# Kernel optimization log

Hardware: AMD Instinct MI355X
Metric: run time of the kernel (lower is better)

The kernel has to match this reference:

```python
import jax, jax.numpy as jnp
import numpy as np

B, T, I = 32768, 28, 28
H, C = 128, 10


def setup_inputs() -> dict:
    key = jax.random.key(0)
    ks = jax.random.split(key, 7)
    s_u = 1.0 / np.sqrt(I)
    s_w = 1.0 / np.sqrt(H)
    return {
        "x": jax.random.normal(ks[0], (B, T, I), dtype=jnp.float32),
        "U_w": jax.random.uniform(ks[1], (H, I), jnp.float32, -s_u, s_u),
        "U_b": jax.random.uniform(ks[2], (H,), jnp.float32, -s_u, s_u),
        "W_w": jax.random.uniform(ks[3], (H, H), jnp.float32, -s_w, s_w),
        "W_b": jax.random.uniform(ks[4], (H,), jnp.float32, -s_w, s_w),
        "V_w": jax.random.uniform(ks[5], (C, H), jnp.float32, -s_w, s_w),
        "V_b": jax.random.uniform(ks[6], (C,), jnp.float32, -s_w, s_w),
    }


def reference(x, U_w, U_b, W_w, W_b, V_w, V_b):
    # x: [B, T, I]. Precompute input projections for all timesteps at once
    # (one big GEMM), then scan the sequential recurrence on S.
    ux = jnp.einsum("bti,hi->tbh", x, U_w) + U_b  # [T, B, H]

    def step(S, ux_t):
        S = jnp.tanh(ux_t + S @ W_w.T + W_b)
        return S, None

    S0 = jnp.zeros((x.shape[0], W_w.shape[0]), dtype=x.dtype)
    S_final, _ = jax.lax.scan(step, S0, ux)
    return S_final @ V_w.T + V_b  # [B, C]
```

## Files before the change

kernel.cpp:

```cpp
#include <hip/hip_runtime.h>


#define T_STEPS 28
#define I_DIM   28
#define S_STRIDE 132

typedef __attribute__((ext_vector_type(4))) float f32x4;
typedef __attribute__((ext_vector_type(8))) short short8;

#define MFMA16 __builtin_amdgcn_mfma_f32_16x16x32_bf16

__device__ __forceinline__ unsigned short f2bf(float f) {
  unsigned u = __builtin_bit_cast(unsigned, f);
  u += 0x7FFFu + ((u >> 16) & 1u);
  return (unsigned short)(u >> 16);
}
__device__ __forceinline__ float bf2f(unsigned short s) {
  return __builtin_bit_cast(float, (unsigned)s << 16);
}

__device__ __forceinline__ short8 to_frag(f32x4 a, f32x4 b) {
  union { unsigned short u[8]; short8 v; } r;
#pragma unroll
  for (int j = 0; j < 4; ++j) { r.u[j] = f2bf(a[j]); r.u[j + 4] = f2bf(b[j]); }
  return r.v;
}

__device__ __forceinline__ short8 load_sfrag(const unsigned short* sp, int off) {
  union { uint2 d[2]; short8 v; } r;
  r.d[0] = *(const uint2*)(sp + off);
  r.d[1] = *(const uint2*)(sp + off + 4);
  return r.v;
}

__device__ __forceinline__ float fast_tanh(float z) {
  float e = __expf(2.0f * z);
#if __has_builtin(__builtin_amdgcn_rcpf)
  return 1.0f - 2.0f * __builtin_amdgcn_rcpf(e + 1.0f);
#else
  return 1.0f - 2.0f / (e + 1.0f);
#endif
}

__global__ __launch_bounds__(256, 2) void rnn_fused(
    const float* __restrict__ x,  const float* __restrict__ Uw,
    const float* __restrict__ Ub, const float* __restrict__ Ww,
    const float* __restrict__ Wb, const float* __restrict__ Vw,
    const float* __restrict__ Vb, float* __restrict__ out) {
  __shared__ unsigned short Sbuf[2][64 * S_STRIDE];

  const int tid  = threadIdx.x;
  const int w    = tid >> 6;
  const int lane = tid & 63;
  const int l15  = lane & 15;
  const int q    = lane >> 4;
  const int mrow = (w >> 1) * 64;
  const int ncol = (w & 1) * 32;
  const int b0   = blockIdx.x * 64;

  const f32x4 zero4 = {0.f, 0.f, 0.f, 0.f};

  short8 wfrag[4][4];
  short8 ufrag[4];
  f32x4  bias[4];
#pragma unroll
  for (int mt = 0; mt < 4; ++mt) {
    const int h = mrow + mt * 16 + l15;
    const float* wp = Ww + h * 128 + q * 8;
#pragma unroll
    for (int kt = 0; kt < 4; ++kt) {
      wfrag[mt][kt] = to_frag(*(const f32x4*)wp, *(const f32x4*)(wp + 4));
      wp += 32;
    }
    const float* up = Uw + h * I_DIM + q * 8;
    f32x4 u0 = *(const f32x4*)up;
    f32x4 u1 = zero4;
    if (q < 3) u1 = *(const f32x4*)(up + 4);
    ufrag[mt] = to_frag(u0, u1);
    const int hb = mrow + mt * 16 + q * 4;
    bias[mt] = *(const f32x4*)(Wb + hb) + *(const f32x4*)(Ub + hb);
  }

  const float* xptr[2];
#pragma unroll
  for (int nt = 0; nt < 2; ++nt)
    xptr[nt] = x + (size_t)(b0 + ncol + nt * 16 + l15) * (T_STEPS * I_DIM) + q * 8;

  int ro[2];
#pragma unroll
  for (int nt = 0; nt < 2; ++nt) ro[nt] = (ncol + nt * 16 + l15) * S_STRIDE;

  f32x4 acc[4][2];

  {
    f32x4 xa[2], xbv[2];
#pragma unroll
    for (int nt = 0; nt < 2; ++nt) {
      xa[nt] = *(const f32x4*)xptr[nt];
      xbv[nt] = zero4;
      if (q < 3) xbv[nt] = *(const f32x4*)(xptr[nt] + 4);
      xptr[nt] += I_DIM;
    }
    short8 xf0 = to_frag(xa[0], xbv[0]);
    short8 xf1 = to_frag(xa[1], xbv[1]);
#pragma unroll
    for (int mt = 0; mt < 4; ++mt) {
      acc[mt][0] = MFMA16(ufrag[mt], xf0, zero4, 0, 0, 0);
      acc[mt][1] = MFMA16(ufrag[mt], xf1, zero4, 0, 0, 0);
    }
    unsigned short* wp = &Sbuf[1][0];
#pragma unroll
    for (int mt = 0; mt < 4; ++mt)
#pragma unroll
      for (int nt = 0; nt < 2; ++nt) {
        f32x4 z = acc[mt][nt] + bias[mt];
        unsigned s0 = f2bf(fast_tanh(z[0]));
        unsigned s1 = f2bf(fast_tanh(z[1]));
        unsigned s2 = f2bf(fast_tanh(z[2]));
        unsigned s3 = f2bf(fast_tanh(z[3]));
        uint2 d; d.x = s0 | (s1 << 16); d.y = s2 | (s3 << 16);
        *(uint2*)(wp + ro[nt] + mrow + mt * 16 + q * 4) = d;
      }
  }
  __syncthreads();

#pragma unroll 1
  for (int t = 1; t < T_STEPS; ++t) {
    f32x4 xa[2], xbv[2];
#pragma unroll
    for (int nt = 0; nt < 2; ++nt) {
      xa[nt] = *(const f32x4*)xptr[nt];
      xbv[nt] = zero4;
      if (q < 3) xbv[nt] = *(const f32x4*)(xptr[nt] + 4);
      xptr[nt] += I_DIM;
    }

    const unsigned short* sp = &Sbuf[t & 1][0];
#pragma unroll
    for (int mt = 0; mt < 4; ++mt) { acc[mt][0] = zero4; acc[mt][1] = zero4; }

#pragma unroll
    for (int kt = 0; kt < 4; ++kt) {
      short8 s0 = load_sfrag(sp, ro[0] + kt * 32 + q * 8);
      short8 s1 = load_sfrag(sp, ro[1] + kt * 32 + q * 8);
#pragma unroll
      for (int mt = 0; mt < 4; ++mt) {
        acc[mt][0] = MFMA16(wfrag[mt][kt], s0, acc[mt][0], 0, 0, 0);
        acc[mt][1] = MFMA16(wfrag[mt][kt], s1, acc[mt][1], 0, 0, 0);
      }
    }

    short8 xf0 = to_frag(xa[0], xbv[0]);
    short8 xf1 = to_frag(xa[1], xbv[1]);
#pragma unroll
    for (int mt = 0; mt < 4; ++mt) {
      acc[mt][0] = MFMA16(ufrag[mt], xf0, acc[mt][0], 0, 0, 0);
      acc[mt][1] = MFMA16(ufrag[mt], xf1, acc[mt][1], 0, 0, 0);
    }

    unsigned short* wp = &Sbuf[(t + 1) & 1][0];
#pragma unroll
    for (int mt = 0; mt < 4; ++mt)
#pragma unroll
      for (int nt = 0; nt < 2; ++nt) {
        f32x4 z = acc[mt][nt] + bias[mt];
        unsigned s0 = f2bf(fast_tanh(z[0]));
        unsigned s1 = f2bf(fast_tanh(z[1]));
        unsigned s2 = f2bf(fast_tanh(z[2]));
        unsigned s3 = f2bf(fast_tanh(z[3]));
        uint2 d; d.x = s0 | (s1 << 16); d.y = s2 | (s3 << 16);
        *(uint2*)(wp + ro[nt] + mrow + mt * 16 + q * 4) = d;
      }
    __syncthreads();
  }

  {
    const unsigned short* sf = &Sbuf[0][0];
    const int r  = tid >> 2;
    const int c0 = tid & 3;
    const float* v0 = Vw + c0 * 128;
    const float* v1 = Vw + (c0 + 4) * 128;
    const float* v2 = Vw + ((c0 & 1) + 8) * 128;
    const unsigned short* srow = sf + r * S_STRIDE;
    float a0 = 0.f, a1 = 0.f, a2 = 0.f;
#pragma unroll 8
    for (int h = 0; h < 128; ++h) {
      float s = bf2f(srow[h]);
      a0 += s * v0[h];
      a1 += s * v1[h];
      a2 += s * v2[h];
    }
    float* op = out + (size_t)(b0 + r) * 10;
    op[c0]     = a0 + Vb[c0];
    op[c0 + 4] = a1 + Vb[c0 + 4];
    if (c0 < 2) op[c0 + 8] = a2 + Vb[c0 + 8];
  }
}

extern "C" void kernel_launch(void* const* d_in, const int* in_sizes, int n_in,
                              void* d_out, int out_size, void* d_ws, size_t ws_size,
                              hipStream_t stream) {
  const float* x  = (const float*)d_in[0];
  const float* Uw = (const float*)d_in[1];
  const float* Ub = (const float*)d_in[2];
  const float* Ww = (const float*)d_in[3];
  const float* Wb = (const float*)d_in[4];
  const float* Vw = (const float*)d_in[5];
  const float* Vb = (const float*)d_in[6];
  rnn_fused<<<512, 256, 0, stream>>>(x, Uw, Ub, Ww, Wb, Vw, Vb, (float*)d_out);
}
```

Baseline: 213.6 us.

## Halve batch tile per block, raise occupancy, use packed bf16 convert and exp2 tanh

Each block now handles 32 batch rows instead of 64 and the grid doubles to 1024 blocks. Launch bounds rise to 4 blocks per CU, so each wave issues fewer MFMAs per recurrence step, and more independent blocks are available to hide barrier and global-load latency. bf16 conversion switches to the packed cvt_pk builtin, tanh uses a vectorised exp2/rcp form, and the bias is folded into the accumulator initialisation. The cost is that the W fragments are reloaded per block for half as many rows, and the tighter register limit risks spills.

```diff
diff --git a/kernel.cpp b/kernel.cpp
--- a/kernel.cpp
+++ b/kernel.cpp
@@ -10,19 +10,29 @@
 
 #define MFMA16 __builtin_amdgcn_mfma_f32_16x16x32_bf16
 
-__device__ __forceinline__ unsigned short f2bf(float f) {
-  unsigned u = __builtin_bit_cast(unsigned, f);
-  u += 0x7FFFu + ((u >> 16) & 1u);
-  return (unsigned short)(u >> 16);
+__device__ __forceinline__ unsigned pack2(float lo, float hi) {
+#if __has_builtin(__builtin_amdgcn_cvt_pk_bf16_f32)
+  auto p = __builtin_amdgcn_cvt_pk_bf16_f32(lo, hi);
+  return __builtin_bit_cast(unsigned, p);
+#else
+  unsigned a = __builtin_bit_cast(unsigned, lo);
+  a += 0x7FFFu + ((a >> 16) & 1u);
+  unsigned b = __builtin_bit_cast(unsigned, hi);
+  b += 0x7FFFu + ((b >> 16) & 1u);
+  return (a >> 16) | (b & 0xFFFF0000u);
+#endif
 }
+
 __device__ __forceinline__ float bf2f(unsigned short s) {
   return __builtin_bit_cast(float, (unsigned)s << 16);
 }
 
 __device__ __forceinline__ short8 to_frag(f32x4 a, f32x4 b) {
-  union { unsigned short u[8]; short8 v; } r;
-#pragma unroll
-  for (int j = 0; j < 4; ++j) { r.u[j] = f2bf(a[j]); r.u[j + 4] = f2bf(b[j]); }
+  union { unsigned u[4]; short8 v; } r;
+  r.u[0] = pack2(a[0], a[1]);
+  r.u[1] = pack2(a[2], a[3]);
+  r.u[2] = pack2(b[0], b[1]);
+  r.u[3] = pack2(b[2], b[3]);
   return r.v;
 }
 
@@ -33,21 +43,25 @@
   return r.v;
 }
 
-__device__ __forceinline__ float fast_tanh(float z) {
-  float e = __expf(2.0f * z);
-#if __has_builtin(__builtin_amdgcn_rcpf)
-  return 1.0f - 2.0f * __builtin_amdgcn_rcpf(e + 1.0f);
-#else
-  return 1.0f - 2.0f / (e + 1.0f);
-#endif
+__device__ __forceinline__ f32x4 tanh4(f32x4 z) {
+  const float k = 2.8853900817779268f;
+  f32x4 t = z * k;
+  f32x4 e;
+#pragma unroll
+  for (int i = 0; i < 4; ++i) e[i] = __builtin_amdgcn_exp2f(t[i]);
+  f32x4 d = e + 1.0f;
+  f32x4 r;
+#pragma unroll
+  for (int i = 0; i < 4; ++i) r[i] = __builtin_amdgcn_rcpf(d[i]);
+  return 1.0f - 2.0f * r;
 }
 
-__global__ __launch_bounds__(256, 2) void rnn_fused(
+__global__ __launch_bounds__(256, 4) void rnn_fused(
     const float* __restrict__ x,  const float* __restrict__ Uw,
     const float* __restrict__ Ub, const float* __restrict__ Ww,
     const float* __restrict__ Wb, const float* __restrict__ Vw,
     const float* __restrict__ Vb, float* __restrict__ out) {
-  __shared__ unsigned short Sbuf[2][64 * S_STRIDE];
+  __shared__ __align__(16) unsigned short Sbuf[2][32 * S_STRIDE];
 
   const int tid  = threadIdx.x;
   const int w    = tid >> 6;
@@ -55,8 +69,8 @@
   const int l15  = lane & 15;
   const int q    = lane >> 4;
   const int mrow = (w >> 1) * 64;
-  const int ncol = (w & 1) * 32;
-  const int b0   = blockIdx.x * 64;
+  const int ncol = (w & 1) * 16;
+  const int b0   = blockIdx.x * 32;
 
   const f32x4 zero4 = {0.f, 0.f, 0.f, 0.f};
 
@@ -81,119 +95,79 @@
     bias[mt] = *(const f32x4*)(Wb + hb) + *(const f32x4*)(Ub + hb);
   }
 
-  const float* xptr[2];
-#pragma unroll
-  for (int nt = 0; nt < 2; ++nt)
-    xptr[nt] = x + (size_t)(b0 + ncol + nt * 16 + l15) * (T_STEPS * I_DIM) + q * 8;
+  const float* xlo = x + (size_t)(b0 + ncol + l15) * (T_STEPS * I_DIM) + q * 8;
+  const float* xhi = x + (size_t)(b0 + ncol + l15) * (T_STEPS * I_DIM)
+                       + ((q < 3) ? q * 8 + 4 : 0);
 
-  int ro[2];
-#pragma unroll
-  for (int nt = 0; nt < 2; ++nt) ro[nt] = (ncol + nt * 16 + l15) * S_STRIDE;
-
-  f32x4 acc[4][2];
+  const int ro = (ncol + l15) * S_STRIDE;
+  f32x4 acc[4];
 
   {
-    f32x4 xa[2], xbv[2];
-#pragma unroll
-    for (int nt = 0; nt < 2; ++nt) {
-      xa[nt] = *(const f32x4*)xptr[nt];
-      xbv[nt] = zero4;
-      if (q < 3) xbv[nt] = *(const f32x4*)(xptr[nt] + 4);
-      xptr[nt] += I_DIM;
-    }
-    short8 xf0 = to_frag(xa[0], xbv[0]);
-    short8 xf1 = to_frag(xa[1], xbv[1]);
+    f32x4 xa = *(const f32x4*)xlo;
+    f32x4 xb = *(const f32x4*)xhi;
+    xlo += I_DIM; xhi += I_DIM;
+    short8 xf = to_frag(xa, xb);
+    unsigned short* wp = &Sbuf[1][0];
 #pragma unroll
     for (int mt = 0; mt < 4; ++mt) {
-      acc[mt][0] = MFMA16(ufrag[mt], xf0, zero4, 0, 0, 0);
-      acc[mt][1] = MFMA16(ufrag[mt], xf1, zero4, 0, 0, 0);
+      acc[mt] = MFMA16(ufrag[mt], xf, bias[mt], 0, 0, 0);
+      f32x4 th = tanh4(acc[mt]);
+      uint2 dd; dd.x = pack2(th[0], th[1]); dd.y = pack2(th[2], th[3]);
+      *(uint2*)(wp + ro + mrow + mt * 16 + q * 4) = dd;
     }
-    unsigned short* wp = &Sbuf[1][0];
-#pragma unroll
-    for (int mt = 0; mt < 4; ++mt)
-#pragma unroll
-      for (int nt = 0; nt < 2; ++nt) {
-        f32x4 z = acc[mt][nt] + bias[mt];
-        unsigned s0 = f2bf(fast_tanh(z[0]));
-        unsigned s1 = f2bf(fast_tanh(z[1]));
-        unsigned s2 = f2bf(fast_tanh(z[2]));
-        unsigned s3 = f2bf(fast_tanh(z[3]));
-        uint2 d; d.x = s0 | (s1 << 16); d.y = s2 | (s3 << 16);
-        *(uint2*)(wp + ro[nt] + mrow + mt * 16 + q * 4) = d;
-      }
   }
   __syncthreads();
 
 #pragma unroll 1
   for (int t = 1; t < T_STEPS; ++t) {
-    f32x4 xa[2], xbv[2];
-#pragma unroll
-    for (int nt = 0; nt < 2; ++nt) {
-      xa[nt] = *(const f32x4*)xptr[nt];
-      xbv[nt] = zero4;
-      if (q < 3) xbv[nt] = *(const f32x4*)(xptr[nt] + 4);
-      xptr[nt] += I_DIM;
-    }
+    f32x4 xa = *(const f32x4*)xlo;
+    f32x4 xb = *(const f32x4*)xhi;
+    xlo += I_DIM; xhi += I_DIM;
 
     const unsigned short* sp = &Sbuf[t & 1][0];
 #pragma unroll
-    for (int mt = 0; mt < 4; ++mt) { acc[mt][0] = zero4; acc[mt][1] = zero4; }
+    for (int mt = 0; mt < 4; ++mt) acc[mt] = bias[mt];
 
 #pragma unroll
     for (int kt = 0; kt < 4; ++kt) {
-      short8 s0 = load_sfrag(sp, ro[0] + kt * 32 + q * 8);
-      short8 s1 = load_sfrag(sp, ro[1] + kt * 32 + q * 8);
+      short8 s0 = load_sfrag(sp, ro + kt * 32 + q * 8);
 #pragma unroll
-      for (int mt = 0; mt < 4; ++mt) {
-        acc[mt][0] = MFMA16(wfrag[mt][kt], s0, acc[mt][0], 0, 0, 0);
-        acc[mt][1] = MFMA16(wfrag[mt][kt], s1, acc[mt][1], 0, 0, 0);
-      }
+      for (int mt = 0; mt < 4; ++mt)
+        acc[mt] = MFMA16(wfrag[mt][kt], s0, acc[mt], 0, 0, 0);
     }
 
-    short8 xf0 = to_frag(xa[0], xbv[0]);
-    short8 xf1 = to_frag(xa[1], xbv[1]);
+    short8 xf = to_frag(xa, xb);
 #pragma unroll
-    for (int mt = 0; mt < 4; ++mt) {
-      acc[mt][0] = MFMA16(ufrag[mt], xf0, acc[mt][0], 0, 0, 0);
-      acc[mt][1] = MFMA16(ufrag[mt], xf1, acc[mt][1], 0, 0, 0);
-    }
+    for (int mt = 0; mt < 4; ++mt)
+      acc[mt] = MFMA16(ufrag[mt], xf, acc[mt], 0, 0, 0);
 
     unsigned short* wp = &Sbuf[(t + 1) & 1][0];
 #pragma unroll
-    for (int mt = 0; mt < 4; ++mt)
-#pragma unroll
-      for (int nt = 0; nt < 2; ++nt) {
-        f32x4 z = acc[mt][nt] + bias[mt];
-        unsigned s0 = f2bf(fast_tanh(z[0]));
-        unsigned s1 = f2bf(fast_tanh(z[1]));
-        unsigned s2 = f2bf(fast_tanh(z[2]));
-        unsigned s3 = f2bf(fast_tanh(z[3]));
-        uint2 d; d.x = s0 | (s1 << 16); d.y = s2 | (s3 << 16);
-        *(uint2*)(wp + ro[nt] + mrow + mt * 16 + q * 4) = d;
-      }
+    for (int mt = 0; mt < 4; ++mt) {
+      f32x4 th = tanh4(acc[mt]);
+      uint2 dd; dd.x = pack2(th[0], th[1]); dd.y = pack2(th[2], th[3]);
+      *(uint2*)(wp + ro + mrow + mt * 16 + q * 4) = dd;
+    }
     __syncthreads();
   }
 
   {
     const unsigned short* sf = &Sbuf[0][0];
-    const int r  = tid >> 2;
-    const int c0 = tid & 3;
+    const int r  = tid >> 3;
+    const int c0 = tid & 7;
     const float* v0 = Vw + c0 * 128;
-    const float* v1 = Vw + (c0 + 4) * 128;
-    const float* v2 = Vw + ((c0 & 1) + 8) * 128;
+    const float* v1 = Vw + ((c0 & 1) + 8) * 128;
     const unsigned short* srow = sf + r * S_STRIDE;
-    float a0 = 0.f, a1 = 0.f, a2 = 0.f;
+    float a0 = 0.f, a1 = 0.f;
 #pragma unroll 8
     for (int h = 0; h < 128; ++h) {
       float s = bf2f(srow[h]);
       a0 += s * v0[h];
       a1 += s * v1[h];
-      a2 += s * v2[h];
     }
     float* op = out + (size_t)(b0 + r) * 10;
-    op[c0]     = a0 + Vb[c0];
-    op[c0 + 4] = a1 + Vb[c0 + 4];
-    if (c0 < 2) op[c0 + 8] = a2 + Vb[c0 + 8];
+    op[c0] = a0 + Vb[c0];
+    if (c0 < 2) op[c0 + 8] = a1 + Vb[(c0 & 1) + 8];
   }
 }
 
@@ -207,5 +181,5 @@
   const float* Wb = (const float*)d_in[4];
   const float* Vw = (const float*)d_in[5];
   const float* Vb = (const float*)d_in[6];
-  rnn_fused<<<512, 256, 0, stream>>>(x, Uw, Ub, Ww, Wb, Vw, Vb, (float*)d_out);
+  rnn_fused<<<1024, 256, 0, stream>>>(x, Uw, Ub, Ww, Wb, Vw, Vb, (float*)d_out);
 }
```

Result: slower. 267.7 us (+25.3%).
